# Optimization experiments

Measured on AMD Instinct MI355X. Metric: run time of the kernel, lower is better.

## Reference

```python
import jax, jax.numpy as jnp
import numpy as np
from jax import lax

EPOCHS = 3
N_IN, N_OUT = 20, 18
BN_EPS = 1e-5
RECT_EPS = 1e-4
TRIU = np.triu_indices(N_OUT)  # SPDVectorize upper-triangular indices


def _orth(key, n, m):
    # Stiefel init: orthonormal columns, like nn.init.orthogonal_
    q, _ = jnp.linalg.qr(jax.random.normal(key, (n, m), dtype=jnp.float32))
    return q


def setup_inputs() -> dict:
    key = jax.random.key(0)
    ks = jax.random.split(key, 8)
    bs = 2048
    f32 = jnp.float32
    return dict(
        x=jax.random.normal(ks[0], (bs, 1, 22, 438), dtype=f32),
        W1=jax.random.normal(ks[1], (22, 1, 22, 1), dtype=f32) * 0.1,
        b1=jnp.zeros((22,), f32),
        g1=jnp.ones((22,), f32), be1=jnp.zeros((22,), f32),
        W2=jax.random.normal(ks[2], (20, 22, 1, 12), dtype=f32) * 0.05,
        b2=jnp.zeros((20,), f32),
        g2=jnp.ones((20,), f32), be2=jnp.zeros((20,), f32),
        Wq=_orth(ks[3], N_IN, N_OUT),
        Wk=_orth(ks[4], N_IN, N_OUT),
        Wv=_orth(ks[5], N_IN, N_OUT),
        Wl=jax.random.normal(ks[6], (N_OUT * (N_OUT + 1) // 2 * EPOCHS, 4), dtype=f32) * 0.02,
        bl=jnp.zeros((4,), f32),
    )


def _bn(x, g, b):
    # BatchNorm2d forward in training mode (batch statistics, biased var)
    mean = x.mean(axis=(0, 2, 3), keepdims=True)
    var = ((x - mean) ** 2).mean(axis=(0, 2, 3), keepdims=True)
    return (x - mean) * lax.rsqrt(var + BN_EPS) * g[None, :, None, None] + b[None, :, None, None]


def _conv(x, w, b, pad_w):
    y = lax.conv_general_dilated(x, w, (1, 1), [(0, 0), (pad_w, pad_w)],
                                 dimension_numbers=('NCHW', 'OIHW', 'NCHW'))
    return y + b[None, :, None, None]


def _signal2spd(x):
    # x: (bs, C, L) -> trace-normalized covariance + 1e-5 * I
    L = x.shape[-1]
    xc = x - x.mean(-1, keepdims=True)
    cov = jnp.einsum('bcl,bdl->bcd', xc, xc) / (L - 1)
    cov = cov / jnp.trace(cov, axis1=-2, axis2=-1)[:, None, None]
    return cov + 1e-5 * jnp.eye(cov.shape[-1], dtype=cov.dtype)


def _patch_lens(n, epochs):
    base = n // epochs
    lens = [base] * epochs
    for i in range(n - base * epochs):
        lens[i] += 1
    return lens


def _spd_fn(t, fn):
    # SPD functional calculus via eigh (== torch.svd on SPD input)
    s, u = jnp.linalg.eigh(t)
    return jnp.einsum('...ij,...j,...kj->...ik', u, fn(s), u)


def _forward(x, W1, b1, g1, be1, W2, b2, g2, be2, Wq, Wk, Wv, Wl, bl):
    bs = x.shape[0]
    h = _bn(_conv(x, W1, b1, 0), g1, be1)          # (bs,22,1,438)
    h = _bn(_conv(h, W2, b2, 6), g2, be2)          # (bs,20,1,439)
    sig = h[:, :, 0, :]                            # squeeze -> (bs,20,439)
    covs, off = [], 0
    for L in _patch_lens(sig.shape[-1], EPOCHS):   # E2R: [147,146,146]
        covs.append(_signal2spd(sig[:, :, off:off + L]))
        off += L
    X = jnp.stack(covs, axis=1)                    # (bs,m,20,20) SPD
    # SPDTransform: W^T X W with Stiefel W (20,18)
    Q = jnp.einsum('pi,bmpq,qj->bmij', Wq, X, Wq)
    K = jnp.einsum('pi,bmpq,qj->bmij', Wk, X, Wk)
    V = jnp.einsum('pi,bmpq,qj->bmij', Wv, X, Wv)
    logQ = _spd_fn(Q, jnp.log)
    logK = _spd_fn(K, jnp.log)
    logV = _spd_fn(V, jnp.log)
    # log-Euclidean distance^2: ||log Q_j - log K_i||_F^2  (== sum of svd singvals of D D^T)
    diff = logQ[:, :, None] - logK[:, None, :]     # (bs, mq, mk, n, n)
    energy = jnp.sum(diff * diff, axis=(-2, -1))   # (bs, mq, mk)
    scores = 1.0 / (1.0 + jnp.log1p(energy))
    # torch: softmax over dim=-2 then permute(0,2,1) == softmax over K index here
    P = jax.nn.softmax(scores, axis=-1)            # (bs, mq, mk)
    mixed = jnp.einsum('bji,bipq->bjpq', P, logV)  # weighted log-Euclidean mean
    out = _spd_fn(mixed, jnp.exp)
    out = _spd_fn(out, lambda s: jnp.maximum(s, RECT_EPS))  # SPDRectified
    logO = _spd_fn(out, jnp.log)                   # SPDTangentSpace log
    vec = logO[..., TRIU[0], TRIU[1]]              # (bs, m, 171)
    return vec.reshape(bs, -1) @ Wl + bl           # (bs, 4)


def reference(x, W1, b1, g1, be1, W2, b2, g2, be2, Wq, Wk, Wv, Wl, bl):
    return _forward(x, W1, b1, g1, be1, W2, b2, g2, be2, Wq, Wk, Wv, Wl, bl)
```

## Files before the change

### kernel.cpp

```cpp
#include <hip/hip_runtime.h>
#include <math.h>

#define OFF_Y2   0
#define OFF_QKV  17981440
#define OFF_ST   (17981440 + 5971968)
#define ST_SX   0
#define ST_SXX  22
#define ST_WF   506
#define ST_BF   990
#define ST_Y2S  1012
#define ST_Y2Q  1032
#define ST_TOT  1052

#define LOGEPS -9.210340371976182f
#define NSWEEP 5
#define SHIFT  12.0f

__global__ __launch_bounds__(256) void k0_zero(float* __restrict__ st){
  for (int i = threadIdx.x; i < ST_TOT; i += 256) st[i] = 0.f;
}

__global__ __launch_bounds__(256) void k1_xstats(const float* __restrict__ x, float* __restrict__ st){
  __shared__ __align__(16) float xs[22*444];
  const float* xb = x + (size_t)blockIdx.x * (22*438);
  for (int i = threadIdx.x; i < 22*444; i += 256){
    int h = i / 444, w = i - h*444;
    xs[i] = (w < 438) ? xb[h*438 + w] : 0.f;
  }
  __syncthreads();
  for (int t = threadIdx.x; t < 275; t += 256){
    if (t < 22){
      const float4* r = (const float4*)&xs[t*444];
      float4 acc = {0.f,0.f,0.f,0.f};
      for (int w = 0; w < 111; ++w){ float4 v = r[w]; acc.x+=v.x; acc.y+=v.y; acc.z+=v.z; acc.w+=v.w; }
      atomicAdd(&st[ST_SX + t], acc.x+acc.y+acc.z+acc.w);
    } else {
      int rem = t - 22, h = 0;
      while (rem >= 22 - h){ rem -= 22 - h; ++h; }
      int h2 = h + rem;
      const float4* ra = (const float4*)&xs[h*444];
      const float4* rb = (const float4*)&xs[h2*444];
      float4 acc = {0.f,0.f,0.f,0.f};
      for (int w = 0; w < 111; ++w){
        float4 a = ra[w], b = rb[w];
        acc.x = fmaf(a.x,b.x,acc.x); acc.y = fmaf(a.y,b.y,acc.y);
        acc.z = fmaf(a.z,b.z,acc.z); acc.w = fmaf(a.w,b.w,acc.w);
      }
      atomicAdd(&st[ST_SXX + h*22 + h2], acc.x+acc.y+acc.z+acc.w);
    }
  }
}

__global__ __launch_bounds__(64) void k1b_fold(const float* __restrict__ W1, const float* __restrict__ g1,
                                               const float* __restrict__ be1, float* __restrict__ st){
  int c = threadIdx.x;
  if (c >= 22) return;
  const float invN = 1.f / (2048.f*438.f);
  float mcol[22];
  float mu0 = 0.f;
  for (int h = 0; h < 22; ++h){ mcol[h] = W1[c*22 + h]; mu0 = fmaf(mcol[h], st[ST_SX + h], mu0); }
  mu0 *= invN;
  float qf = 0.f;
  for (int h = 0; h < 22; ++h)
    for (int h2 = h; h2 < 22; ++h2){
      float w = mcol[h]*mcol[h2]*st[ST_SXX + h*22 + h2];
      qf += (h2 == h) ? w : 2.f*w;
    }
  qf *= invN;
  float var = qf - mu0*mu0;
  float a1 = g1[c] * rsqrtf(var + 1e-5f);
  for (int h = 0; h < 22; ++h) st[ST_WF + h*22 + c] = a1 * mcol[h];
  st[ST_BF + c] = be1[c] - a1 * mu0;
}

__global__ __launch_bounds__(256) void k2_weff(const float* __restrict__ W2, const float* __restrict__ st,
                                               float* __restrict__ weff, float* __restrict__ pfx){
  __shared__ float wf[484];
  __shared__ float bf[22];
  for (int i = threadIdx.x; i < 484; i += 256) wf[i] = st[ST_WF + i];
  if (threadIdx.x < 22) bf[threadIdx.x] = st[ST_BF + threadIdx.x];
  __syncthreads();
  for (int i = threadIdx.x; i < 5280; i += 256){
    int d = i / 264, r = i - d*264, h = r / 12, t = r - h*12;
    float a = 0.f;
    for (int c = 0; c < 22; ++c) a = fmaf(W2[d*264 + c*12 + t], wf[h*22 + c], a);
    weff[i] = a;
  }
  if (threadIdx.x < 20){
    int d = threadIdx.x;
    float run = 0.f;
    pfx[d*13 + 0] = 0.f;
    for (int t = 0; t < 12; ++t){
      float a = 0.f;
      for (int c = 0; c < 22; ++c) a = fmaf(W2[d*264 + c*12 + t], bf[c], a);
      run += a;
      pfx[d*13 + t + 1] = run;
    }
  }
}

__global__ __launch_bounds__(512, 6) void k3_conv(const float* __restrict__ x,
    const float* __restrict__ weff, const float* __restrict__ pfx,
    float* __restrict__ st, float* __restrict__ y2){
  __shared__ __align__(16) float xs[22*452];
  __shared__ float ps[260];
  __shared__ float sloc[20], qloc[20];
  int tid = threadIdx.x;
  int n = blockIdx.x;
  const float* xb = x + (size_t)n*9636;
  for (int i = tid; i < 22*452; i += 512){
    int h = i / 452, w = i - h*452;
    int gx = w - 6;
    xs[i] = (gx >= 0 && gx < 438) ? xb[h*438 + gx] : 0.f;
  }
  if (tid < 260) ps[tid] = pfx[tid];
  if (tid < 40){ if (tid < 20) sloc[tid] = 0.f; else qloc[tid-20] = 0.f; }
  __syncthreads();
  bool act = tid < 439;
  int gw = act ? tid : 0;
  float acc[20];
  #pragma unroll
  for (int d = 0; d < 20; ++d) acc[d] = 0.f;
  #pragma unroll 1
  for (int h = 0; h < 22; ++h){
    const float* xr = &xs[h*452 + gw];
    float xw[12];
    #pragma unroll
    for (int t = 0; t < 12; ++t) xw[t] = xr[t];
    const float* wp = weff + h*12;
    #pragma unroll
    for (int d = 0; d < 20; ++d){
      const float* wr = wp + d*264;
      #pragma unroll
      for (int t = 0; t < 12; ++t)
        acc[d] = fmaf(wr[t], xw[t], acc[d]);
    }
  }
  int lo = 6 - gw; if (lo < 0) lo = 0;
  int hi = 444 - gw; if (hi > 12) hi = 12;
  float* yb = y2 + (size_t)n*8780 + gw;
  #pragma unroll
  for (int d = 0; d < 20; ++d){
    float val = acc[d] + (ps[d*13 + hi] - ps[d*13 + lo]);
    float sv = act ? val : 0.f;
    float qv = act ? val*val : 0.f;
    if (act) yb[(size_t)d*439] = val;
    #pragma unroll
    for (int off = 32; off; off >>= 1){ sv += __shfl_down(sv, off); qv += __shfl_down(qv, off); }
    if ((tid & 63) == 0){ atomicAdd(&sloc[d], sv); atomicAdd(&qloc[d], qv); }
  }
  __syncthreads();
  if (tid < 20){
    atomicAdd(&st[ST_Y2S + tid], sloc[tid]);
    atomicAdd(&st[ST_Y2Q + tid], qloc[tid]);
  }
}

__global__ __launch_bounds__(256) void k4_cov_qkv(const float* __restrict__ y2, const float* __restrict__ st,
    const float* __restrict__ g2, const float* __restrict__ Wq, const float* __restrict__ Wk,
    const float* __restrict__ Wv, float* __restrict__ qkv){
  __shared__ __align__(16) float ysp[3][20][148];
  __shared__ float a2s[20];
  __shared__ __align__(16) float Bt[3][18][20];
  __shared__ __align__(16) float G3[3][400];
  __shared__ __align__(16) float Tmt[3][360];
  __shared__ float musum3[3][20];
  __shared__ float rtr3[3];
  int tid = threadIdx.x, n = blockIdx.x;
  if (tid < 20){
    const float invN = 1.f/(2048.f*439.f);
    float s = st[ST_Y2S + tid]*invN;
    float q = st[ST_Y2Q + tid]*invN;
    a2s[tid] = g2[tid] * rsqrtf(q - s*s + 1e-5f);
  }
  const float* yb = y2 + (size_t)n*8780;
  for (int i = tid; i < 8780; i += 256){
    int d = i/439, w = i - d*439;
    int m = (w >= 293) ? 2 : ((w >= 147) ? 1 : 0);
    int lw = w - ((m == 2) ? 293 : ((m == 1) ? 147 : 0));
    ysp[m][d][lw] = yb[i];
  }
  if (tid < 100){
    int d = tid/5, k = tid - d*5;
    int m = (k == 0) ? 0 : ((k < 3) ? 1 : 2);
    int lw = (k == 0) ? 147 : ((k == 1 || k == 3) ? 146 : 147);
    ysp[m][d][lw] = 0.f;
  }
  __syncthreads();
  for (int i = tid; i < 1140; i += 256){
    if (i < 1080){
      int wt = i/360, r = i - wt*360; int d = r/18, jj = r - d*18;
      const float* Wm = (wt==0) ? Wq : ((wt==1) ? Wk : Wv);
      Bt[wt][jj][d] = a2s[d]*Wm[d*18 + jj];
    } else {
      int t = i - 1080; int m = t/20, d = t - m*20;
      const float4* r = (const float4*)&ysp[m][d][0];
      float4 acc = {0.f,0.f,0.f,0.f};
      #pragma unroll 1
      for (int w = 0; w < 37; ++w){ float4 v = r[w]; acc.x+=v.x; acc.y+=v.y; acc.z+=v.z; acc.w+=v.w; }
      musum3[m][d] = acc.x+acc.y+acc.z+acc.w;
    }
  }
  __syncthreads();
  for (int it = tid; it < 630; it += 256){
    int m = it/210, t = it - m*210;
    int rem = t, c = 0;
    while (rem >= 20 - c){ rem -= 20 - c; ++c; }
    int d = c + rem;
    const float4* ra = (const float4*)&ysp[m][c][0];
    const float4* rb = (const float4*)&ysp[m][d][0];
    float4 acc4 = {0.f,0.f,0.f,0.f};
    #pragma unroll 1
    for (int w = 0; w < 37; ++w){
      float4 a = ra[w], b = rb[w];
      acc4.x = fmaf(a.x,b.x,acc4.x); acc4.y = fmaf(a.y,b.y,acc4.y);
      acc4.z = fmaf(a.z,b.z,acc4.z); acc4.w = fmaf(a.w,b.w,acc4.w);
    }
    float invL = (m == 0) ? (1.f/147.f) : (1.f/146.f);
    float acc = (acc4.x+acc4.y+acc4.z+acc4.w) - musum3[m][c]*musum3[m][d]*invL;
    G3[m][c*20 + d] = acc; G3[m][d*20 + c] = acc;
  }
  __syncthreads();
  for (int wt = 0; wt < 3; ++wt){
    for (int i = tid; i < 1083; i += 256){
      if (i < 1080){
        int m = i/360, r = i - m*360; int p = r/18, jj = r - p*18;
        const float4* gr = (const float4*)&G3[m][p*20];
        const float4* br = (const float4*)&Bt[wt][jj][0];
        float4 a4 = {0.f,0.f,0.f,0.f};
        #pragma unroll
        for (int w = 0; w < 5; ++w){
          float4 a = gr[w], b = br[w];
          a4.x = fmaf(a.x,b.x,a4.x); a4.y = fmaf(a.y,b.y,a4.y);
          a4.z = fmaf(a.z,b.z,a4.z); a4.w = fmaf(a.w,b.w,a4.w);
        }
        Tmt[m][jj*20 + p] = a4.x+a4.y+a4.z+a4.w;
      } else if (wt == 0){
        int m = i - 1080;
        float tr = 0.f;
        for (int c = 0; c < 20; ++c){ float a = a2s[c]; tr = fmaf(a*a, G3[m][c*21], tr); }
        rtr3[m] = 1.f/tr;
      }
    }
    __syncthreads();
    for (int it = tid; it < 513; it += 256){
      int m = it/171, t = it - m*171;
      int rem = t, i = 0;
      while (rem >= 18 - i){ rem -= 18 - i; ++i; }
      int jj = i + rem;
      const float4* br = (const float4*)&Bt[wt][i][0];
      const float4* tr = (const float4*)&Tmt[m][jj*20];
      float4 a4 = {0.f,0.f,0.f,0.f};
      #pragma unroll
      for (int w = 0; w < 5; ++w){
        float4 a = br[w], b = tr[w];
        a4.x = fmaf(a.x,b.x,a4.x); a4.y = fmaf(a.y,b.y,a4.y);
        a4.z = fmaf(a.z,b.z,a4.z); a4.w = fmaf(a.w,b.w,a4.w);
      }
      float acc = (a4.x+a4.y+a4.z+a4.w) * rtr3[m];
      if (i == jj) acc += 1e-5f;
      float* outm = qkv + ((size_t)wt*6144 + (size_t)n*3 + m)*324;
      outm[i*18 + jj] = acc; outm[jj*18 + i] = acc;
    }
    __syncthreads();
  }
}

__global__ __launch_bounds__(256, 4) void k5_oneside(const float* __restrict__ src, float* __restrict__ dst,
    int nmat, int mode, const float* __restrict__ Wl, const float* __restrict__ bl,
    float* __restrict__ outp){
  __shared__ __align__(16) float stage[12][384];
  __shared__ __align__(16) float wls[2052];
  __shared__ float outacc[4][4];
  int tid = threadIdx.x;
  int wave = tid >> 6, lane = tid & 63;
  int g = (lane >= 54) ? 3 : (lane >= 36 ? 2 : (lane >= 18 ? 1 : 0));
  int j = lane - g*18;
  int gb = g*18;
  int slot = wave*3 + ((g < 3) ? g : 0);
  int mat = blockIdx.x*12 + wave*3 + g;
  bool act = (g < 3) && (mat < nmat);

  if (mode == 1){
    for (int i = tid; i < 2052; i += 256) wls[i] = Wl[i];
    if (tid < 16) outacc[tid >> 2][tid & 3] = 0.f;
  }

  float b[18];
  float sh = (mode == 1) ? SHIFT : 0.f;
  if (act){
    const float* s = src + (size_t)mat*324 + j*18;
    #pragma unroll
    for (int i = 0; i < 18; ++i) b[i] = s[i] + ((i == j) ? sh : 0.f);
  } else {
    #pragma unroll
    for (int i = 0; i < 18; ++i) b[i] = (i == j) ? 1.f : 0.f;
  }
  float nrm;
  { float n0 = 0.f, n1 = 0.f;
    #pragma unroll
    for (int k = 0; k < 18; k += 2){ n0 = fmaf(b[k],b[k],n0); n1 = fmaf(b[k+1],b[k+1],n1); }
    nrm = n0 + n1; }

  #pragma unroll 1
  for (int sweep = 0; sweep < NSWEEP; ++sweep){
    #pragma unroll
    for (int r = 0; r < 17; ++r){
      int xx = j - 1 - r; if (xx < 0) xx += 17;
      int v = r + 17 - xx; if (v >= 17) v -= 17;
      int m = (j == 0) ? (1 + r) : ((xx == 0) ? 0 : (1 + v));
      bool isp = (j == 0) ? true : ((xx == 0) ? false : (xx <= 8));
      int plane = (gb + m) & 63;
      float rv[18];
      #pragma unroll
      for (int k = 0; k < 18; ++k) rv[k] = __shfl(b[k], plane);
      float on = __shfl(nrm, plane);
      float g0 = 0.f, g1 = 0.f;
      #pragma unroll
      for (int k = 0; k < 18; k += 2){ g0 = fmaf(b[k], rv[k], g0); g1 = fmaf(b[k+1], rv[k+1], g1); }
      float gam = g0 + g1;
      float alpha = isp ? nrm : on;
      float beta  = isp ? on  : nrm;
      float tau = (beta - alpha) * 0.5f * __builtin_amdgcn_rcpf(gam);
      float tt = __builtin_amdgcn_rcpf(fabsf(tau) + sqrtf(fmaf(tau, tau, 1.f)));
      float t = (tau >= 0.f) ? tt : -tt;
      if (!(fabsf(gam) > 1e-36f)) t = 0.f;
      float c = __builtin_amdgcn_rsqf(fmaf(t, t, 1.f));
      float s = t*c;
      nrm = fmaf(isp ? -t : t, gam, nrm);
      float sg = isp ? -s : s;
      #pragma unroll
      for (int k = 0; k < 18; ++k) b[k] = fmaf(c, b[k], sg*rv[k]);
    }
  }
  float n0 = 0.f, n1 = 0.f;
  #pragma unroll
  for (int k = 0; k < 18; k += 2){ n0 = fmaf(b[k],b[k],n0); n1 = fmaf(b[k+1],b[k+1],n1); }
  float nf = fmaxf(n0 + n1, 1e-30f);
  float fv = (mode == 0) ? (0.5f * logf(nf)) : fmaxf(sqrtf(nf) - SHIFT, LOGEPS);
  float wv = fv * __builtin_amdgcn_rcpf(nf);
  float* sp = &stage[slot][0];
  if (act){
    #pragma unroll
    for (int k = 0; k < 18; ++k) sp[k*20 + j] = b[k];
    sp[360 + j] = wv;
  }
  __syncthreads();
  if (act){
    float wr[18];
    #pragma unroll
    for (int i = 0; i < 18; ++i) wr[i] = sp[j*20 + i] * sp[360 + i];
    float frow[18];
    #pragma unroll
    for (int i2 = 0; i2 < 18; ++i2){
      const float* br = &sp[i2*20];
      float a0 = 0.f;
      #pragma unroll
      for (int k = 0; k < 16; k += 4){
        float4 v4 = *(const float4*)&br[k];
        a0 = fmaf(wr[k],   v4.x, a0); a0 = fmaf(wr[k+1], v4.y, a0);
        a0 = fmaf(wr[k+2], v4.z, a0); a0 = fmaf(wr[k+3], v4.w, a0);
      }
      a0 = fmaf(wr[16], br[16], a0);
      a0 = fmaf(wr[17], br[17], a0);
      frow[i2] = a0;
    }
    if (mode == 0){
      float* orow = dst + (size_t)mat*324 + j*18;
      #pragma unroll
      for (int i2 = 0; i2 < 18; ++i2) orow[i2] = frow[i2];
    } else {
      int base = (g*171 + j*(37 - j)/2 - j)*4;
      float o0=0.f, o1=0.f, o2=0.f, o3=0.f;
      #pragma unroll
      for (int jj = 0; jj < 18; ++jj){
        if (jj >= j){
          const float* w4 = &wls[base + jj*4];
          o0 = fmaf(frow[jj], w4[0], o0);
          o1 = fmaf(frow[jj], w4[1], o1);
          o2 = fmaf(frow[jj], w4[2], o2);
          o3 = fmaf(frow[jj], w4[3], o3);
        }
      }
      atomicAdd(&outacc[wave][0], o0);
      atomicAdd(&outacc[wave][1], o1);
      atomicAdd(&outacc[wave][2], o2);
      atomicAdd(&outacc[wave][3], o3);
    }
  }
  if (mode == 1){
    __syncthreads();
    if (tid < 16){
      int bi = tid >> 2, o = tid & 3;
      outp[(blockIdx.x*4 + bi)*4 + o] = outacc[bi][o] + bl[o];
    }
  }
}

__global__ __launch_bounds__(128) void k6_attnmix(const float* __restrict__ logs, float* __restrict__ mixed){
  __shared__ float lq[972], lk[972], lv[972];
  __shared__ float ew[2][9];
  __shared__ float P[9];
  int b = blockIdx.x, tid = threadIdx.x;
  const float* q  = logs + (size_t)b*972;
  const float* k_ = logs + 1990656 + (size_t)b*972;
  const float* v_ = logs + 3981312 + (size_t)b*972;
  for (int i = tid; i < 972; i += 128){ lq[i] = q[i]; lk[i] = k_[i]; lv[i] = v_[i]; }
  __syncthreads();
  float e[9] = {0.f,0.f,0.f,0.f,0.f,0.f,0.f,0.f,0.f};
  for (int x = tid; x < 324; x += 128){
    float q0 = lq[x], q1 = lq[324+x], q2 = lq[648+x];
    float k0 = lk[x], k1 = lk[324+x], k2 = lk[648+x];
    float d;
    d = q0-k0; e[0] = fmaf(d,d,e[0]);
    d = q0-k1; e[1] = fmaf(d,d,e[1]);
    d = q0-k2; e[2] = fmaf(d,d,e[2]);
    d = q1-k0; e[3] = fmaf(d,d,e[3]);
    d = q1-k1; e[4] = fmaf(d,d,e[4]);
    d = q1-k2; e[5] = fmaf(d,d,e[5]);
    d = q2-k0; e[6] = fmaf(d,d,e[6]);
    d = q2-k1; e[7] = fmaf(d,d,e[7]);
    d = q2-k2; e[8] = fmaf(d,d,e[8]);
  }
  #pragma unroll
  for (int p = 0; p < 9; ++p)
    for (int off = 32; off; off >>= 1) e[p] += __shfl_down(e[p], off);
  if ((tid & 63) == 0){
    #pragma unroll
    for (int p = 0; p < 9; ++p) ew[tid >> 6][p] = e[p];
  }
  __syncthreads();
  if (tid < 3){
    float en0 = ew[0][tid*3+0] + ew[1][tid*3+0];
    float en1 = ew[0][tid*3+1] + ew[1][tid*3+1];
    float en2 = ew[0][tid*3+2] + ew[1][tid*3+2];
    float s0 = 1.f/(1.f + log1pf(en0));
    float s1 = 1.f/(1.f + log1pf(en1));
    float s2 = 1.f/(1.f + log1pf(en2));
    float mx = fmaxf(s0, fmaxf(s1, s2));
    float e0 = expf(s0-mx), e1 = expf(s1-mx), e2 = expf(s2-mx);
    float inv = 1.f/(e0+e1+e2);
    P[tid*3+0] = e0*inv; P[tid*3+1] = e1*inv; P[tid*3+2] = e2*inv;
  }
  __syncthreads();
  float p00=P[0],p01=P[1],p02=P[2],p10=P[3],p11=P[4],p12=P[5],p20=P[6],p21=P[7],p22=P[8];
  float* mb = mixed + (size_t)b*972;
  for (int x = tid; x < 324; x += 128){
    float v0 = lv[x], v1 = lv[324+x], v2 = lv[648+x];
    mb[x]     = p00*v0 + p01*v1 + p02*v2;
    mb[324+x] = p10*v0 + p11*v1 + p12*v2;
    mb[648+x] = p20*v0 + p21*v1 + p22*v2;
  }
}

extern "C" void kernel_launch(void* const* d_in, const int* in_sizes, int n_in,
                              void* d_out, int out_size, void* d_ws, size_t ws_size,
                              hipStream_t stream){
  (void)in_sizes; (void)n_in; (void)out_size; (void)ws_size;
  const float* x   = (const float*)d_in[0];
  const float* W1  = (const float*)d_in[1];
  const float* g1  = (const float*)d_in[3];
  const float* be1 = (const float*)d_in[4];
  const float* W2  = (const float*)d_in[5];
  const float* g2  = (const float*)d_in[7];
  const float* Wq  = (const float*)d_in[9];
  const float* Wk  = (const float*)d_in[10];
  const float* Wv  = (const float*)d_in[11];
  const float* Wl  = (const float*)d_in[12];
  const float* bl  = (const float*)d_in[13];
  float* ws    = (float*)d_ws;
  float* y2    = ws + OFF_Y2;
  float* qkv   = ws + OFF_QKV;
  float* weff  = ws + OFF_QKV;
  float* pfx   = ws + OFF_QKV + 5280;
  float* logs  = ws + OFF_Y2;
  float* mixed = ws + OFF_QKV;
  float* st    = ws + OFF_ST;
  float* outp  = (float*)d_out;

  k0_zero    <<<dim3(1),       dim3(256), 0, stream>>>(st);
  k1_xstats  <<<dim3(2048),    dim3(256), 0, stream>>>(x, st);
  k1b_fold   <<<dim3(1),       dim3(64),  0, stream>>>(W1, g1, be1, st);
  k2_weff    <<<dim3(1),       dim3(256), 0, stream>>>(W2, st, weff, pfx);
  k3_conv    <<<dim3(2048),    dim3(512), 0, stream>>>(x, weff, pfx, st, y2);
  k4_cov_qkv <<<dim3(2048),    dim3(256), 0, stream>>>(y2, st, g2, Wq, Wk, Wv, qkv);
  k5_oneside <<<dim3(1536),    dim3(256), 0, stream>>>(qkv, logs, 18432, 0, nullptr, nullptr, nullptr);
  k6_attnmix <<<dim3(2048),    dim3(128), 0, stream>>>(logs, mixed);
  k5_oneside <<<dim3(512),     dim3(256), 0, stream>>>(mixed, nullptr, 6144, 1, Wl, bl, outp);
}
```

Baseline: 776.1 us.

## Register-tile conv by output group and four columns per thread

The conv kernel now splits its 512 threads into four output-channel groups of five channels each. Every thread computes four adjacent output columns using float4 shared-memory loads, so each loaded x value and each weight is reused across several FMAs. The weight layout is reordered per group so a wave reads contiguous, wave-uniform weights. Per-thread registers grow (20 accumulators plus a 16-wide window), so the occupancy hint drops from 6 to 3 blocks per CU, and about 14% of lanes sit idle.

Result: faster. 659.4 us (-15.0%).

```diff
diff --git a/kernel.cpp b/kernel.cpp
--- a/kernel.cpp
+++ b/kernel.cpp
@@ -74,17 +74,20 @@
 }
 
 __global__ __launch_bounds__(256) void k2_weff(const float* __restrict__ W2, const float* __restrict__ st,
-                                               float* __restrict__ weff, float* __restrict__ pfx){
+                                               float* __restrict__ weff2, float* __restrict__ pfx){
   __shared__ float wf[484];
   __shared__ float bf[22];
   for (int i = threadIdx.x; i < 484; i += 256) wf[i] = st[ST_WF + i];
   if (threadIdx.x < 22) bf[threadIdx.x] = st[ST_BF + threadIdx.x];
   __syncthreads();
   for (int i = threadIdx.x; i < 5280; i += 256){
-    int d = i / 264, r = i - d*264, h = r / 12, t = r - h*12;
+    int t = i % 12; int tmp = i / 12;
+    int dl = tmp % 5; tmp /= 5;
+    int h = tmp % 22; int dg = tmp / 22;
+    int d = dg*5 + dl;
     float a = 0.f;
     for (int c = 0; c < 22; ++c) a = fmaf(W2[d*264 + c*12 + t], wf[h*22 + c], a);
-    weff[i] = a;
+    weff2[i] = a;
   }
   if (threadIdx.x < 20){
     int d = threadIdx.x;
@@ -99,8 +102,8 @@
   }
 }
 
-__global__ __launch_bounds__(512, 6) void k3_conv(const float* __restrict__ x,
-    const float* __restrict__ weff, const float* __restrict__ pfx,
+__global__ __launch_bounds__(512, 3) void k3_conv(const float* __restrict__ x,
+    const float* __restrict__ weff2, const float* __restrict__ pfx,
     float* __restrict__ st, float* __restrict__ y2){
   __shared__ __align__(16) float xs[22*452];
   __shared__ float ps[260];
@@ -116,38 +119,70 @@
   if (tid < 260) ps[tid] = pfx[tid];
   if (tid < 40){ if (tid < 20) sloc[tid] = 0.f; else qloc[tid-20] = 0.f; }
   __syncthreads();
-  bool act = tid < 439;
-  int gw = act ? tid : 0;
-  float acc[20];
+  int wave = tid >> 6;
+  int dg = __builtin_amdgcn_readfirstlane(wave >> 1);
+  int ct = tid & 127;
+  bool act = ct < 110;
+  int c0 = act ? ct*4 : 0;
+  float acc[5][4];
   #pragma unroll
-  for (int d = 0; d < 20; ++d) acc[d] = 0.f;
+  for (int dl = 0; dl < 5; ++dl)
+    #pragma unroll
+    for (int j = 0; j < 4; ++j) acc[dl][j] = 0.f;
+  const float* wb = weff2 + dg*1320;
   #pragma unroll 1
   for (int h = 0; h < 22; ++h){
-    const float* xr = &xs[h*452 + gw];
-    float xw[12];
-    #pragma unroll
-    for (int t = 0; t < 12; ++t) xw[t] = xr[t];
-    const float* wp = weff + h*12;
-    #pragma unroll
-    for (int d = 0; d < 20; ++d){
-      const float* wr = wp + d*264;
-      #pragma unroll
-      for (int t = 0; t < 12; ++t)
-        acc[d] = fmaf(wr[t], xw[t], acc[d]);
-    }
-  }
-  int lo = 6 - gw; if (lo < 0) lo = 0;
-  int hi = 444 - gw; if (hi > 12) hi = 12;
-  float* yb = y2 + (size_t)n*8780 + gw;
+    const float4* xr = (const float4*)&xs[h*452 + c0];
+    float4 v0 = xr[0], v1 = xr[1], v2 = xr[2], v3 = xr[3];
+    float xw[16] = {v0.x,v0.y,v0.z,v0.w, v1.x,v1.y,v1.z,v1.w,
+                    v2.x,v2.y,v2.z,v2.w, v3.x,v3.y,v3.z,v3.w};
+    const float* wp = wb + h*60;
+    #pragma unroll
+    for (int dl = 0; dl < 5; ++dl){
+      #pragma unroll
+      for (int t = 0; t < 12; ++t){
+        float w = wp[dl*12 + t];
+        #pragma unroll
+        for (int j = 0; j < 4; ++j)
+          acc[dl][j] = fmaf(w, xw[t+j], acc[dl][j]);
+      }
+    }
+  }
+  float s5[5], q5[5];
   #pragma unroll
-  for (int d = 0; d < 20; ++d){
-    float val = acc[d] + (ps[d*13 + hi] - ps[d*13 + lo]);
-    float sv = act ? val : 0.f;
-    float qv = act ? val*val : 0.f;
-    if (act) yb[(size_t)d*439] = val;
-    #pragma unroll
-    for (int off = 32; off; off >>= 1){ sv += __shfl_down(sv, off); qv += __shfl_down(qv, off); }
-    if ((tid & 63) == 0){ atomicAdd(&sloc[d], sv); atomicAdd(&qloc[d], qv); }
+  for (int dl = 0; dl < 5; ++dl){ s5[dl] = 0.f; q5[dl] = 0.f; }
+  if (act){
+    #pragma unroll
+    for (int dl = 0; dl < 5; ++dl){
+      int d = dg*5 + dl;
+      float* yb = y2 + (size_t)n*8780 + (size_t)d*439;
+      #pragma unroll
+      for (int j = 0; j < 4; ++j){
+        int gw = c0 + j;
+        if (gw < 439){
+          int lo = 6 - gw; if (lo < 0) lo = 0;
+          int hi = 444 - gw; if (hi > 12) hi = 12;
+          float val = acc[dl][j] + (ps[d*13 + hi] - ps[d*13 + lo]);
+          yb[gw] = val;
+          s5[dl] += val; q5[dl] = fmaf(val, val, q5[dl]);
+        }
+      }
+    }
+  }
+  #pragma unroll
+  for (int off = 32; off; off >>= 1){
+    #pragma unroll
+    for (int dl = 0; dl < 5; ++dl){
+      s5[dl] += __shfl_down(s5[dl], off);
+      q5[dl] += __shfl_down(q5[dl], off);
+    }
+  }
+  if ((tid & 63) == 0){
+    #pragma unroll
+    for (int dl = 0; dl < 5; ++dl){
+      atomicAdd(&sloc[dg*5 + dl], s5[dl]);
+      atomicAdd(&qloc[dg*5 + dl], q5[dl]);
+    }
   }
   __syncthreads();
   if (tid < 20){
@@ -471,7 +506,7 @@
   float* ws    = (float*)d_ws;
   float* y2    = ws + OFF_Y2;
   float* qkv   = ws + OFF_QKV;
-  float* weff  = ws + OFF_QKV;
+  float* weff2 = ws + OFF_QKV;
   float* pfx   = ws + OFF_QKV + 5280;
   float* logs  = ws + OFF_Y2;
   float* mixed = ws + OFF_QKV;
@@ -481,8 +516,8 @@
   k0_zero    <<<dim3(1),       dim3(256), 0, stream>>>(st);
   k1_xstats  <<<dim3(2048),    dim3(256), 0, stream>>>(x, st);
   k1b_fold   <<<dim3(1),       dim3(64),  0, stream>>>(W1, g1, be1, st);
-  k2_weff    <<<dim3(1),       dim3(256), 0, stream>>>(W2, st, weff, pfx);
-  k3_conv    <<<dim3(2048),    dim3(512), 0, stream>>>(x, weff, pfx, st, y2);
+  k2_weff    <<<dim3(1),       dim3(256), 0, stream>>>(W2, st, weff2, pfx);
+  k3_conv    <<<dim3(2048),    dim3(512), 0, stream>>>(x, weff2, pfx, st, y2);
   k4_cov_qkv <<<dim3(2048),    dim3(256), 0, stream>>>(y2, st, g2, Wq, Wk, Wv, qkv);
   k5_oneside <<<dim3(1536),    dim3(256), 0, stream>>>(qkv, logs, 18432, 0, nullptr, nullptr, nullptr);
   k6_attnmix <<<dim3(2048),    dim3(128), 0, stream>>>(logs, mixed);
```
